# Performance work log

Measured on AMD Instinct MI355X. Metric: run time of the kernel, lower is better.

The kernel has to match this reference:

```python
import jax, jax.numpy as jnp
import numpy as np

H = 56; W = 56; WS = 7; SS = 3; NH = 6; C = 192; B = 32
T = H * W; HD = C // NH; NW = (H // WS) * (W // WS); TW = WS * WS
SCALE = HD ** -0.5


def _rel_index():
    # relative position index per WindowAttentionLayer.calculate_coordinates
    coords = np.stack(np.meshgrid(np.arange(WS), np.arange(WS), indexing='ij')).reshape(2, -1)
    rel = (coords[:, :, None] - coords[:, None, :]).transpose(1, 2, 0).astype(np.int64)
    rel[:, :, 0] += WS - 1
    rel[:, :, 1] += WS - 1
    rel[:, :, 0] *= 2 * WS - 1
    return rel.sum(-1).reshape(-1)  # [TW*TW]


def _attn_mask():
    # shifted-window attention mask, per WindowAttentionBlock.__init__
    img = np.zeros((H, W))
    slices = (slice(0, -WS), slice(-WS, -SS), slice(-SS, None))
    cnt = 0
    for hs in slices:
        for ws_ in slices:
            img[hs, ws_] = cnt
            cnt += 1
    mw = img.reshape(H // WS, WS, W // WS, WS).transpose(0, 2, 1, 3).reshape(-1, TW)
    am = mw[:, None, :] - mw[:, :, None]
    return np.where(am != 0, np.float32(-100.0), np.float32(0.0))  # [NW, TW, TW]


_REL = jnp.asarray(_rel_index())
_MASK = jnp.asarray(_attn_mask())


def _ln(x, g, b):
    m = x.mean(-1, keepdims=True)
    v = ((x - m) ** 2).mean(-1, keepdims=True)
    return (x - m) * jax.lax.rsqrt(v + 1e-5) * g + b


def setup_inputs() -> dict:
    key = jax.random.key(0)
    ks = jax.random.split(key, 8)
    s = 0.02
    return {
        'x': jax.random.normal(ks[0], (B, T, C), jnp.float32),
        'ln1_g': jnp.ones((C,), jnp.float32),
        'ln1_b': jnp.zeros((C,), jnp.float32),
        'qkv_w': jax.random.normal(ks[1], (C, 3 * C), jnp.float32) * s,
        'qkv_b': jnp.zeros((3 * C,), jnp.float32),
        'pos_bias': jax.random.normal(ks[2], ((2 * WS - 1) * (2 * WS - 1), NH), jnp.float32) * s,
        'proj_w': jax.random.normal(ks[3], (C, C), jnp.float32) * s,
        'proj_b': jnp.zeros((C,), jnp.float32),
        'ln2_g': jnp.ones((C,), jnp.float32),
        'ln2_b': jnp.zeros((C,), jnp.float32),
        'mlp_w1': jax.random.normal(ks[4], (C, 4 * C), jnp.float32) * s,
        'mlp_b1': jnp.zeros((4 * C,), jnp.float32),
        'mlp_w2': jax.random.normal(ks[5], (4 * C, C), jnp.float32) * s,
        'mlp_b2': jnp.zeros((C,), jnp.float32),
    }


def reference(x, ln1_g, ln1_b, qkv_w, qkv_b, pos_bias, proj_w, proj_b,
              ln2_g, ln2_b, mlp_w1, mlp_b1, mlp_w2, mlp_b2):
    shortcut = x
    h = _ln(x, ln1_g, ln1_b).reshape(B, H, W, C)
    h = jnp.roll(h, (-SS, -SS), axis=(1, 2))  # cyclic shift
    # window partition -> [B*NW, TW, C]
    h = h.reshape(B, H // WS, WS, W // WS, WS, C).transpose(0, 1, 3, 2, 4, 5).reshape(B * NW, TW, C)
    qkv = (h @ qkv_w + qkv_b).reshape(B * NW, TW, 3, NH, HD).transpose(2, 0, 3, 1, 4)
    q, k, v = qkv[0] * SCALE, qkv[1], qkv[2]  # [B*NW, NH, TW, HD]
    attn = jnp.einsum('nhid,nhjd->nhij', q, k)  # [B*NW, NH, TW, TW]
    bias = pos_bias[_REL].reshape(TW, TW, NH).transpose(2, 0, 1)  # [NH, TW, TW]
    attn = attn + bias[None]
    attn = (attn.reshape(B, NW, NH, TW, TW) + _MASK[None, :, None]).reshape(B * NW, NH, TW, TW)
    # NOTE: the source forward never applies softmax (self.softmax is unused) -- replicated faithfully
    o = jnp.einsum('nhij,nhjd->nhid', attn, v).transpose(0, 2, 1, 3).reshape(B * NW, TW, C)
    o = o @ proj_w + proj_b
    # window reverse + reverse shift
    o = o.reshape(B, H // WS, W // WS, WS, WS, C).transpose(0, 1, 3, 2, 4, 5).reshape(B, H, W, C)
    o = jnp.roll(o, (SS, SS), axis=(1, 2)).reshape(B, T, C)
    x1 = shortcut + o
    m = _ln(x1, ln2_g, ln2_b)
    m = jax.nn.gelu(m @ mlp_w1 + mlp_b1, approximate=False) @ mlp_w2 + mlp_b2
    return x1 + m
```

## Files before the change

kernel.cpp:

```cpp
#include <hip/hip_runtime.h>
#include <hip/hip_bf16.h>

typedef __attribute__((ext_vector_type(8))) short short8;
typedef __attribute__((ext_vector_type(4))) float floatx4;

#define SCALE_Q 0.17677669529663687f

__device__ __forceinline__ short f2bf(float f) {
  union { float f; unsigned u; } a; a.f = f;
  unsigned r = (a.u + 0x7FFFu + ((a.u >> 16) & 1u)) >> 16;
  return (short)r;
}

__device__ __forceinline__ int spatial_row(int r) {
  int n = r / 49, tw = r - n * 49;
  int bb = n >> 6, wdx = n & 63;
  int rh = (wdx >> 3) * 7 + tw / 7, rw = (wdx & 7) * 7 + tw % 7;
  int oh = rh + 3; if (oh >= 56) oh -= 56;
  int ow = rw + 3; if (ow >= 56) ow -= 56;
  return bb * 3136 + oh * 56 + ow;
}

__global__ void transpose_w_k(const float* __restrict__ src, short* __restrict__ dst,
                              int K, int N) {
  int i = blockIdx.x * 256 + threadIdx.x;
  if (i >= N * K) return;
  int n = i / K, k = i - n * K;
  dst[i] = f2bf(src[(size_t)k * N + n]);
}

__global__ void prep_bm_k(const float* __restrict__ pos_bias, float* __restrict__ bm) {
  int i = blockIdx.x * 256 + threadIdx.x;
  if (i >= 64 * 6 * 49 * 49) return;
  int j = i % 49; int t = i / 49; int ii = t % 49; t /= 49; int h = t % 6; int w = t / 6;
  int ih = ii / 7, iw = ii - ih * 7, jh = j / 7, jw = j - jh * 7;
  int rel = (ih - jh + 6) * 13 + (iw - jw + 6);
  float v = pos_bias[rel * 6 + h];
  int wh = w >> 3, ww = w & 7;
  int ri = wh * 7 + ih, ci = ww * 7 + iw, rj = wh * 7 + jh, cj = ww * 7 + jw;
  int regi = ((ri >= 49) + (ri >= 53)) * 3 + ((ci >= 49) + (ci >= 53));
  int regj = ((rj >= 49) + (rj >= 53)) * 3 + ((cj >= 49) + (cj >= 53));
  if (regi != regj) v -= 100.0f;
  bm[i] = v;
}

__global__ __launch_bounds__(256) void ln_k(const float* __restrict__ x,
    const float* __restrict__ g, const float* __restrict__ bta,
    short* __restrict__ outb) {
  int wid = threadIdx.x >> 6, lane = threadIdx.x & 63;
  int r = blockIdx.x * 4 + wid;
  int n = r / 49, tw = r - n * 49;
  int bb = n >> 6, wdx = n & 63;
  int rh = (wdx >> 3) * 7 + tw / 7, rw = (wdx & 7) * 7 + tw % 7;
  int sh = rh + 3; if (sh >= 56) sh -= 56;
  int sw = rw + 3; if (sw >= 56) sw -= 56;
  size_t src = ((size_t)bb * 3136 + sh * 56 + sw) * 192;
  const float* xr = x + src;
  float v0 = xr[lane], v1 = xr[lane + 64], v2 = xr[lane + 128];
  float s = v0 + v1 + v2, sq = v0 * v0 + v1 * v1 + v2 * v2;
  #pragma unroll
  for (int o = 32; o >= 1; o >>= 1) { s += __shfl_xor(s, o); sq += __shfl_xor(sq, o); }
  float mean = s * (1.0f / 192.0f);
  float rstd = rsqrtf(sq * (1.0f / 192.0f) - mean * mean + 1e-5f);
  short* orow = outb + (size_t)r * 192;
  orow[lane]       = f2bf((v0 - mean) * rstd * g[lane]       + bta[lane]);
  orow[lane + 64]  = f2bf((v1 - mean) * rstd * g[lane + 64]  + bta[lane + 64]);
  orow[lane + 128] = f2bf((v2 - mean) * rstd * g[lane + 128] + bta[lane + 128]);
}

__global__ __launch_bounds__(256) void gemm_qkv_k(
    const short* __restrict__ A, const short* __restrict__ Bt,
    const float* __restrict__ bias, short* __restrict__ outp, int N, int K) {
  __shared__ short As[128][72];
  __shared__ short Bs[64][72];
  int tid = threadIdx.x;
  int gmb = blockIdx.y * 128;
  int gnb = blockIdx.x * 64;
  int wid = tid >> 6, lane = tid & 63;
  int wm = wid >> 1, wn = wid & 1;
  int lr = lane & 15, lk = (lane >> 4) << 3, lq = (lane >> 4) << 2;
  floatx4 acc[4][2];
  #pragma unroll
  for (int i = 0; i < 4; ++i)
    #pragma unroll
    for (int j = 0; j < 2; ++j) acc[i][j] = (floatx4)(0.0f);

  for (int k0 = 0; k0 < K; k0 += 64) {
    #pragma unroll
    for (int i = 0; i < 4; ++i) {
      int u = tid + 256 * i;
      int row = u >> 3, cb = (u & 7) << 3;
      *(short8*)&As[row][cb] = *(const short8*)&A[(size_t)(gmb + row) * K + k0 + cb];
    }
    #pragma unroll
    for (int i = 0; i < 2; ++i) {
      int u = tid + 256 * i;
      int row = u >> 3, cb = (u & 7) << 3;
      *(short8*)&Bs[row][cb] = *(const short8*)&Bt[(size_t)(gnb + row) * K + k0 + cb];
    }
    __syncthreads();
    #pragma unroll
    for (int kk = 0; kk < 64; kk += 32) {
      short8 af[4], bfr[2];
      #pragma unroll
      for (int mi = 0; mi < 4; ++mi)
        af[mi] = *(const short8*)&As[wm * 64 + mi * 16 + lr][kk + lk];
      #pragma unroll
      for (int ni = 0; ni < 2; ++ni)
        bfr[ni] = *(const short8*)&Bs[wn * 32 + ni * 16 + lr][kk + lk];
      #pragma unroll
      for (int mi = 0; mi < 4; ++mi)
        #pragma unroll
        for (int ni = 0; ni < 2; ++ni)
          acc[mi][ni] = __builtin_amdgcn_mfma_f32_16x16x32_bf16(af[mi], bfr[ni], acc[mi][ni], 0, 0, 0);
    }
    __syncthreads();
  }

  #pragma unroll
  for (int mi = 0; mi < 4; ++mi)
    #pragma unroll
    for (int ni = 0; ni < 2; ++ni)
      #pragma unroll
      for (int r = 0; r < 4; ++r) {
        int grow = gmb + wm * 64 + mi * 16 + lq + r;
        int gcol = gnb + wn * 32 + ni * 16 + lr;
        float v = acc[mi][ni][r] + bias[gcol];
        int which = gcol / 192, rem = gcol - which * 192;
        if (which == 0) v *= SCALE_Q;
        int head = rem >> 5, d = rem & 31;
        int n = grow / 49, tw = grow - n * 49;
        outp[((((size_t)(n * 6 + head) * 3 + which) * 49 + tw) << 5) + d] = f2bf(v);
      }
}

__global__ __launch_bounds__(256) void attn_k(const short* __restrict__ qkv,
    const float* __restrict__ bm, short* __restrict__ obuf) {
  __shared__ short lds[4][6912];
  int wid = threadIdx.x >> 6, lane = threadIdx.x & 63;
  int pair = blockIdx.x * 4 + wid;
  int n = pair / 6, h = pair - n * 6;
  short* Vt = &lds[wid][0];
  short* Ps = &lds[wid][32 * 72];
  const short* Qb = qkv + (size_t)((n * 6 + h) * 3) * 1568;
  const short* Kb = Qb + 1568;
  const short* Vb = Qb + 3136;
  int lr = lane & 15, lk = (lane >> 4) << 3, lq = (lane >> 4) << 2;

  #pragma unroll
  for (int it = 0; it < 8; ++it) {
    int u = lane + 64 * it;
    Vt[(u >> 4) * 72 + 48 + (u & 15)] = 0;
  }
  #pragma unroll
  for (int it = 0; it < 4; ++it) {
    int u = lane + 64 * it;
    if (u < 196) {
      int tw = u >> 2, db = (u & 3) << 3;
      short8 vv = *(const short8*)&Vb[tw * 32 + db];
      #pragma unroll
      for (int j = 0; j < 8; ++j) Vt[(db + j) * 72 + tw] = vv[j];
    }
  }

  short8 qf[4], kf[4];
  #pragma unroll
  for (int mi = 0; mi < 4; ++mi)
    qf[mi] = *(const short8*)&Qb[(mi * 16 + lr) * 32 + lk];
  #pragma unroll
  for (int nj = 0; nj < 4; ++nj)
    kf[nj] = *(const short8*)&Kb[(nj * 16 + lr) * 32 + lk];
  floatx4 s[4][4];
  #pragma unroll
  for (int mi = 0; mi < 4; ++mi)
    #pragma unroll
    for (int nj = 0; nj < 4; ++nj)
      s[mi][nj] = __builtin_amdgcn_mfma_f32_16x16x32_bf16(qf[mi], kf[nj], (floatx4)(0.0f), 0, 0, 0);

  const float* bmw = bm + (size_t)((n & 63) * 6 + h) * 2401;
  #pragma unroll
  for (int mi = 0; mi < 4; ++mi)
    #pragma unroll
    for (int nj = 0; nj < 4; ++nj)
      #pragma unroll
      for (int r = 0; r < 4; ++r) {
        int i = mi * 16 + lq + r;
        int j = nj * 16 + lr;
        float v = 0.0f;
        if (i < 49 && j < 49) v = s[mi][nj][r] + bmw[i * 49 + j];
        Ps[i * 72 + j] = f2bf(v);
      }

  floatx4 o[4][2];
  #pragma unroll
  for (int mi = 0; mi < 4; ++mi)
    #pragma unroll
    for (int ni = 0; ni < 2; ++ni) o[mi][ni] = (floatx4)(0.0f);
  #pragma unroll
  for (int kc = 0; kc < 2; ++kc) {
    short8 pf[4], vf[2];
    #pragma unroll
    for (int mi = 0; mi < 4; ++mi)
      pf[mi] = *(const short8*)&Ps[(mi * 16 + lr) * 72 + kc * 32 + lk];
    #pragma unroll
    for (int ni = 0; ni < 2; ++ni)
      vf[ni] = *(const short8*)&Vt[(ni * 16 + lr) * 72 + kc * 32 + lk];
    #pragma unroll
    for (int mi = 0; mi < 4; ++mi)
      #pragma unroll
      for (int ni = 0; ni < 2; ++ni)
        o[mi][ni] = __builtin_amdgcn_mfma_f32_16x16x32_bf16(pf[mi], vf[ni], o[mi][ni], 0, 0, 0);
  }
  #pragma unroll
  for (int mi = 0; mi < 4; ++mi)
    #pragma unroll
    for (int ni = 0; ni < 2; ++ni)
      #pragma unroll
      for (int r = 0; r < 4; ++r) {
        int i = mi * 16 + lq + r;
        if (i < 49)
          obuf[((size_t)n * 49 + i) * 192 + h * 32 + ni * 16 + lr] = f2bf(o[mi][ni][r]);
      }
}

__global__ __launch_bounds__(512, 2) void tail_k(
    const short* __restrict__ obuf, const short* __restrict__ projT,
    const float* __restrict__ proj_b, const float* __restrict__ x,
    const float* __restrict__ g2, const float* __restrict__ bt2,
    const short* __restrict__ w1T, const float* __restrict__ b1,
    const short* __restrict__ w2T, const float* __restrict__ b2,
    float* __restrict__ out) {
  __shared__ short As[128][200];
  __shared__ short Hc[128][72];
  __shared__ float sums[128][4][2];
  __shared__ float stats[128][2];

  int tid = threadIdx.x;
  int wid = tid >> 6, lane = tid & 63;
  int wm = wid >> 2, wn = wid & 3;
  int lr = lane & 15, lk = (lane >> 4) << 3, lq = (lane >> 4) << 2;
  int blk = blockIdx.x * 128;

  floatx4 acc[4][3];
  #pragma unroll
  for (int mi = 0; mi < 4; ++mi)
    #pragma unroll
    for (int ni = 0; ni < 3; ++ni) acc[mi][ni] = (floatx4)(0.0f);
  #pragma unroll
  for (int kk = 0; kk < 6; ++kk) {
    short8 af[4], bfr[3];
    #pragma unroll
    for (int mi = 0; mi < 4; ++mi)
      af[mi] = *(const short8*)&obuf[(size_t)(blk + wm * 64 + mi * 16 + lr) * 192 + kk * 32 + lk];
    #pragma unroll
    for (int ni = 0; ni < 3; ++ni)
      bfr[ni] = *(const short8*)&projT[(size_t)(wn * 48 + ni * 16 + lr) * 192 + kk * 32 + lk];
    #pragma unroll
    for (int mi = 0; mi < 4; ++mi)
      #pragma unroll
      for (int ni = 0; ni < 3; ++ni)
        acc[mi][ni] = __builtin_amdgcn_mfma_f32_16x16x32_bf16(af[mi], bfr[ni], acc[mi][ni], 0, 0, 0);
  }

  float pb[3], gv[3], bv[3], pb2[3];
  int col[3];
  #pragma unroll
  for (int ni = 0; ni < 3; ++ni) {
    col[ni] = wn * 48 + ni * 16 + lr;
    pb[ni] = proj_b[col[ni]];
    gv[ni] = g2[col[ni]];
    bv[ni] = bt2[col[ni]];
    pb2[ni] = b2[col[ni]];
  }

  int srw[4][4];
  #pragma unroll
  for (int mi = 0; mi < 4; ++mi) {
    #pragma unroll
    for (int rr = 0; rr < 4; ++rr) {
      int row_l = wm * 64 + mi * 16 + lq + rr;
      int sr = spatial_row(blk + row_l);
      srw[mi][rr] = sr;
      float s = 0.0f, sq = 0.0f;
      #pragma unroll
      for (int ni = 0; ni < 3; ++ni) {
        float v = acc[mi][ni][rr] + pb[ni] + x[(size_t)sr * 192 + col[ni]];
        acc[mi][ni][rr] = v;
        s += v; sq += v * v;
      }
      #pragma unroll
      for (int o = 8; o >= 1; o >>= 1) { s += __shfl_xor(s, o); sq += __shfl_xor(sq, o); }
      if (lr == 0) { sums[row_l][wn][0] = s; sums[row_l][wn][1] = sq; }
    }
  }
  __syncthreads();
  if (tid < 128) {
    float s = sums[tid][0][0] + sums[tid][1][0] + sums[tid][2][0] + sums[tid][3][0];
    float sq = sums[tid][0][1] + sums[tid][1][1] + sums[tid][2][1] + sums[tid][3][1];
    float mean = s * (1.0f / 192.0f);
    float var = sq * (1.0f / 192.0f) - mean * mean;
    stats[tid][0] = mean;
    stats[tid][1] = rsqrtf(var + 1e-5f);
  }
  __syncthreads();

  #pragma unroll
  for (int mi = 0; mi < 4; ++mi)
    #pragma unroll
    for (int rr = 0; rr < 4; ++rr) {
      int row_l = wm * 64 + mi * 16 + lq + rr;
      float mean = stats[row_l][0], rstd = stats[row_l][1];
      #pragma unroll
      for (int ni = 0; ni < 3; ++ni)
        As[row_l][col[ni]] = f2bf((acc[mi][ni][rr] - mean) * rstd * gv[ni] + bv[ni]);
    }
  __syncthreads();

  int hcol = wn * 16 + lr;
  for (int c = 0; c < 12; ++c) {
    floatx4 hacc[4];
    #pragma unroll
    for (int mi = 0; mi < 4; ++mi) hacc[mi] = (floatx4)(0.0f);
    const short* w1p = w1T + (size_t)(c * 64 + hcol) * 192;
    #pragma unroll
    for (int kk = 0; kk < 6; ++kk) {
      short8 bfr = *(const short8*)&w1p[kk * 32 + lk];
      short8 af[4];
      #pragma unroll
      for (int mi = 0; mi < 4; ++mi)
        af[mi] = *(const short8*)&As[wm * 64 + mi * 16 + lr][kk * 32 + lk];
      #pragma unroll
      for (int mi = 0; mi < 4; ++mi)
        hacc[mi] = __builtin_amdgcn_mfma_f32_16x16x32_bf16(af[mi], bfr, hacc[mi], 0, 0, 0);
    }
    float b1v = b1[c * 64 + hcol];
    #pragma unroll
    for (int mi = 0; mi < 4; ++mi)
      #pragma unroll
      for (int rr = 0; rr < 4; ++rr) {
        float hv = hacc[mi][rr] + b1v;
        float ge = 0.5f * hv * (1.0f + erff(hv * 0.70710678118f));
        Hc[wm * 64 + mi * 16 + lq + rr][hcol] = f2bf(ge);
      }
    __syncthreads();
    #pragma unroll
    for (int kk = 0; kk < 2; ++kk) {
      short8 af[4], bfr[3];
      #pragma unroll
      for (int mi = 0; mi < 4; ++mi)
        af[mi] = *(const short8*)&Hc[wm * 64 + mi * 16 + lr][kk * 32 + lk];
      #pragma unroll
      for (int ni = 0; ni < 3; ++ni)
        bfr[ni] = *(const short8*)&w2T[(size_t)col[ni] * 768 + c * 64 + kk * 32 + lk];
      #pragma unroll
      for (int mi = 0; mi < 4; ++mi)
        #pragma unroll
        for (int ni = 0; ni < 3; ++ni)
          acc[mi][ni] = __builtin_amdgcn_mfma_f32_16x16x32_bf16(af[mi], bfr[ni], acc[mi][ni], 0, 0, 0);
    }
    __syncthreads();
  }

  #pragma unroll
  for (int mi = 0; mi < 4; ++mi)
    #pragma unroll
    for (int rr = 0; rr < 4; ++rr) {
      int sr = srw[mi][rr];
      #pragma unroll
      for (int ni = 0; ni < 3; ++ni)
        out[(size_t)sr * 192 + col[ni]] = acc[mi][ni][rr] + pb2[ni];
    }
}

extern "C" void kernel_launch(void* const* d_in, const int* in_sizes, int n_in,
                              void* d_out, int out_size, void* d_ws, size_t ws_size,
                              hipStream_t stream) {
  const float* x      = (const float*)d_in[0];
  const float* ln1_g  = (const float*)d_in[1];
  const float* ln1_b  = (const float*)d_in[2];
  const float* qkv_w  = (const float*)d_in[3];
  const float* qkv_b  = (const float*)d_in[4];
  const float* pos_b  = (const float*)d_in[5];
  const float* proj_w = (const float*)d_in[6];
  const float* proj_b = (const float*)d_in[7];
  const float* ln2_g  = (const float*)d_in[8];
  const float* ln2_b  = (const float*)d_in[9];
  const float* mlp_w1 = (const float*)d_in[10];
  const float* mlp_b1 = (const float*)d_in[11];
  const float* mlp_w2 = (const float*)d_in[12];
  const float* mlp_b2 = (const float*)d_in[13];

  char* ws = (char*)d_ws;
  short* qkvbuf  = (short*)(ws);
  short* obuf    = (short*)(ws + 115605504);
  short* hbuf    = (short*)(ws + 154140672);
  short* wT      = (short*)(ws + 192675840);
  short* qkv_wT  = wT;
  short* proj_wT = wT + 110592;
  short* m1_wT   = wT + 110592 + 36864;
  short* m2_wT   = wT + 110592 + 36864 + 147456;
  float* bm      = (float*)(ws + 193560576);
  float* xout    = (float*)d_out;

  transpose_w_k<<<(110592 + 255) / 256, 256, 0, stream>>>(qkv_w,  qkv_wT, 192, 576);
  transpose_w_k<<<(36864  + 255) / 256, 256, 0, stream>>>(proj_w, proj_wT, 192, 192);
  transpose_w_k<<<(147456 + 255) / 256, 256, 0, stream>>>(mlp_w1, m1_wT,  192, 768);
  transpose_w_k<<<(147456 + 255) / 256, 256, 0, stream>>>(mlp_w2, m2_wT,  768, 192);
  prep_bm_k<<<(64 * 6 * 2401 + 255) / 256, 256, 0, stream>>>(pos_b, bm);

  ln_k<<<25088, 256, 0, stream>>>(x, ln1_g, ln1_b, hbuf);
  gemm_qkv_k<<<dim3(9, 784), 256, 0, stream>>>(hbuf, qkv_wT, qkv_b, qkvbuf, 576, 192);
  attn_k<<<3072, 256, 0, stream>>>(qkvbuf, bm, obuf);
  tail_k<<<784, 512, 0, stream>>>(obuf, proj_wT, proj_b, x, ln2_g, ln2_b,
                                  m1_wT, mlp_b1, m2_wT, mlp_b2, xout);
}
```

Measured before the change: 576.3 us.

## Split fused tail into proj+LN2 kernel and a separate MLP kernel

Breaks the single tail kernel (proj GEMM, residual, LN2, MLP) into two kernels. The first writes x1 in fp32 to the output and a bf16 LN2 result into the workspace, reusing the qkv buffer. The second runs the MLP over 64-row tiles with 256-thread blocks and adds the residual back into the output. The aim is higher occupancy and better wave balance from smaller blocks and more of them. The cost is an extra round trip to global memory for x1 and the LN2 activations, and the MLP rows are now in spatial order rather than window order.

```diff
diff --git a/kernel.cpp b/kernel.cpp
--- a/kernel.cpp
+++ b/kernel.cpp
@@ -223,67 +223,61 @@
       }
 }
 
-__global__ __launch_bounds__(512, 2) void tail_k(
+__global__ __launch_bounds__(256, 4) void proj_ln2_k(
     const short* __restrict__ obuf, const short* __restrict__ projT,
     const float* __restrict__ proj_b, const float* __restrict__ x,
     const float* __restrict__ g2, const float* __restrict__ bt2,
-    const short* __restrict__ w1T, const float* __restrict__ b1,
-    const short* __restrict__ w2T, const float* __restrict__ b2,
-    float* __restrict__ out) {
-  __shared__ short As[128][200];
-  __shared__ short Hc[128][72];
-  __shared__ float sums[128][4][2];
-  __shared__ float stats[128][2];
-
+    float* __restrict__ x1out, short* __restrict__ ln2out) {
+  __shared__ float sums[64][2][2];
+  __shared__ float stats[64][2];
   int tid = threadIdx.x;
   int wid = tid >> 6, lane = tid & 63;
-  int wm = wid >> 2, wn = wid & 3;
+  int wm = wid >> 1, wn = wid & 1;
   int lr = lane & 15, lk = (lane >> 4) << 3, lq = (lane >> 4) << 2;
-  int blk = blockIdx.x * 128;
-
-  floatx4 acc[4][3];
-  #pragma unroll
-  for (int mi = 0; mi < 4; ++mi)
-    #pragma unroll
-    for (int ni = 0; ni < 3; ++ni) acc[mi][ni] = (floatx4)(0.0f);
+  int R0 = blockIdx.x * 64;
+
+  floatx4 acc[2][6];
+  #pragma unroll
+  for (int mi = 0; mi < 2; ++mi)
+    #pragma unroll
+    for (int ni = 0; ni < 6; ++ni) acc[mi][ni] = (floatx4)(0.0f);
+
   #pragma unroll
   for (int kk = 0; kk < 6; ++kk) {
-    short8 af[4], bfr[3];
-    #pragma unroll
-    for (int mi = 0; mi < 4; ++mi)
-      af[mi] = *(const short8*)&obuf[(size_t)(blk + wm * 64 + mi * 16 + lr) * 192 + kk * 32 + lk];
-    #pragma unroll
-    for (int ni = 0; ni < 3; ++ni)
-      bfr[ni] = *(const short8*)&projT[(size_t)(wn * 48 + ni * 16 + lr) * 192 + kk * 32 + lk];
-    #pragma unroll
-    for (int mi = 0; mi < 4; ++mi)
-      #pragma unroll
-      for (int ni = 0; ni < 3; ++ni)
+    short8 af[2], bfr[6];
+    #pragma unroll
+    for (int mi = 0; mi < 2; ++mi)
+      af[mi] = *(const short8*)&obuf[(size_t)(R0 + wm * 32 + mi * 16 + lr) * 192 + kk * 32 + lk];
+    #pragma unroll
+    for (int ni = 0; ni < 6; ++ni)
+      bfr[ni] = *(const short8*)&projT[(size_t)(wn * 96 + ni * 16 + lr) * 192 + kk * 32 + lk];
+    #pragma unroll
+    for (int mi = 0; mi < 2; ++mi)
+      #pragma unroll
+      for (int ni = 0; ni < 6; ++ni)
         acc[mi][ni] = __builtin_amdgcn_mfma_f32_16x16x32_bf16(af[mi], bfr[ni], acc[mi][ni], 0, 0, 0);
   }
 
-  float pb[3], gv[3], bv[3], pb2[3];
-  int col[3];
-  #pragma unroll
-  for (int ni = 0; ni < 3; ++ni) {
-    col[ni] = wn * 48 + ni * 16 + lr;
+  int col[6]; float pb[6], gv[6], bv[6];
+  #pragma unroll
+  for (int ni = 0; ni < 6; ++ni) {
+    col[ni] = wn * 96 + ni * 16 + lr;
     pb[ni] = proj_b[col[ni]];
     gv[ni] = g2[col[ni]];
     bv[ni] = bt2[col[ni]];
-    pb2[ni] = b2[col[ni]];
-  }
-
-  int srw[4][4];
-  #pragma unroll
-  for (int mi = 0; mi < 4; ++mi) {
+  }
+
+  int srw[2][4];
+  #pragma unroll
+  for (int mi = 0; mi < 2; ++mi)
     #pragma unroll
     for (int rr = 0; rr < 4; ++rr) {
-      int row_l = wm * 64 + mi * 16 + lq + rr;
-      int sr = spatial_row(blk + row_l);
+      int row_l = wm * 32 + mi * 16 + lq + rr;
+      int sr = spatial_row(R0 + row_l);
       srw[mi][rr] = sr;
       float s = 0.0f, sq = 0.0f;
       #pragma unroll
-      for (int ni = 0; ni < 3; ++ni) {
+      for (int ni = 0; ni < 6; ++ni) {
         float v = acc[mi][ni][rr] + pb[ni] + x[(size_t)sr * 192 + col[ni]];
         acc[mi][ni][rr] = v;
         s += v; sq += v * v;
@@ -292,11 +286,10 @@
       for (int o = 8; o >= 1; o >>= 1) { s += __shfl_xor(s, o); sq += __shfl_xor(sq, o); }
       if (lr == 0) { sums[row_l][wn][0] = s; sums[row_l][wn][1] = sq; }
     }
-  }
   __syncthreads();
-  if (tid < 128) {
-    float s = sums[tid][0][0] + sums[tid][1][0] + sums[tid][2][0] + sums[tid][3][0];
-    float sq = sums[tid][0][1] + sums[tid][1][1] + sums[tid][2][1] + sums[tid][3][1];
+  if (tid < 64) {
+    float s = sums[tid][0][0] + sums[tid][1][0];
+    float sq = sums[tid][0][1] + sums[tid][1][1];
     float mean = s * (1.0f / 192.0f);
     float var = sq * (1.0f / 192.0f) - mean * mean;
     stats[tid][0] = mean;
@@ -305,70 +298,116 @@
   __syncthreads();
 
   #pragma unroll
-  for (int mi = 0; mi < 4; ++mi)
+  for (int mi = 0; mi < 2; ++mi)
     #pragma unroll
     for (int rr = 0; rr < 4; ++rr) {
-      int row_l = wm * 64 + mi * 16 + lq + rr;
+      int row_l = wm * 32 + mi * 16 + lq + rr;
+      int sr = srw[mi][rr];
       float mean = stats[row_l][0], rstd = stats[row_l][1];
       #pragma unroll
-      for (int ni = 0; ni < 3; ++ni)
-        As[row_l][col[ni]] = f2bf((acc[mi][ni][rr] - mean) * rstd * gv[ni] + bv[ni]);
-    }
+      for (int ni = 0; ni < 6; ++ni) {
+        float v = acc[mi][ni][rr];
+        x1out[(size_t)sr * 192 + col[ni]] = v;
+        ln2out[(size_t)sr * 192 + col[ni]] = f2bf((v - mean) * rstd * gv[ni] + bv[ni]);
+      }
+    }
+}
+
+__global__ __launch_bounds__(256, 4) void mlp_k(
+    const short* __restrict__ ln2b, const float* __restrict__ x1,
+    const short* __restrict__ w1T, const float* __restrict__ b1,
+    const short* __restrict__ w2T, const float* __restrict__ b2,
+    float* __restrict__ out) {
+  __shared__ short As[64][200];
+  __shared__ short Hc[64][72];
+  int tid = threadIdx.x;
+  int wid = tid >> 6, lane = tid & 63;
+  int wm = wid >> 1, wn = wid & 1;
+  int lr = lane & 15, lk = (lane >> 4) << 3, lq = (lane >> 4) << 2;
+  int R0 = blockIdx.x * 64;
+
+  #pragma unroll
+  for (int it = 0; it < 6; ++it) {
+    int u = tid + 256 * it;
+    int row = u / 24, cb = (u - row * 24) * 8;
+    *(short8*)&As[row][cb] = *(const short8*)&ln2b[(size_t)(R0 + row) * 192 + cb];
+  }
+
+  float b2v[6];
+  int col[6];
+  #pragma unroll
+  for (int ni = 0; ni < 6; ++ni) {
+    col[ni] = wn * 96 + ni * 16 + lr;
+    b2v[ni] = b2[col[ni]];
+  }
+
+  floatx4 acc[2][6];
+  #pragma unroll
+  for (int mi = 0; mi < 2; ++mi)
+    #pragma unroll
+    for (int ni = 0; ni < 6; ++ni) acc[mi][ni] = (floatx4)(0.0f);
   __syncthreads();
 
-  int hcol = wn * 16 + lr;
   for (int c = 0; c < 12; ++c) {
-    floatx4 hacc[4];
-    #pragma unroll
-    for (int mi = 0; mi < 4; ++mi) hacc[mi] = (floatx4)(0.0f);
-    const short* w1p = w1T + (size_t)(c * 64 + hcol) * 192;
+    floatx4 hacc[2][2];
+    #pragma unroll
+    for (int mi = 0; mi < 2; ++mi)
+      #pragma unroll
+      for (int si = 0; si < 2; ++si) hacc[mi][si] = (floatx4)(0.0f);
     #pragma unroll
     for (int kk = 0; kk < 6; ++kk) {
-      short8 bfr = *(const short8*)&w1p[kk * 32 + lk];
-      short8 af[4];
-      #pragma unroll
-      for (int mi = 0; mi < 4; ++mi)
-        af[mi] = *(const short8*)&As[wm * 64 + mi * 16 + lr][kk * 32 + lk];
-      #pragma unroll
-      for (int mi = 0; mi < 4; ++mi)
-        hacc[mi] = __builtin_amdgcn_mfma_f32_16x16x32_bf16(af[mi], bfr, hacc[mi], 0, 0, 0);
-    }
-    float b1v = b1[c * 64 + hcol];
-    #pragma unroll
-    for (int mi = 0; mi < 4; ++mi)
-      #pragma unroll
-      for (int rr = 0; rr < 4; ++rr) {
-        float hv = hacc[mi][rr] + b1v;
-        float ge = 0.5f * hv * (1.0f + erff(hv * 0.70710678118f));
-        Hc[wm * 64 + mi * 16 + lq + rr][hcol] = f2bf(ge);
-      }
+      short8 af[2], bf1[2];
+      #pragma unroll
+      for (int mi = 0; mi < 2; ++mi)
+        af[mi] = *(const short8*)&As[wm * 32 + mi * 16 + lr][kk * 32 + lk];
+      #pragma unroll
+      for (int si = 0; si < 2; ++si)
+        bf1[si] = *(const short8*)&w1T[(size_t)(c * 64 + wn * 32 + si * 16 + lr) * 192 + kk * 32 + lk];
+      #pragma unroll
+      for (int mi = 0; mi < 2; ++mi)
+        #pragma unroll
+        for (int si = 0; si < 2; ++si)
+          hacc[mi][si] = __builtin_amdgcn_mfma_f32_16x16x32_bf16(af[mi], bf1[si], hacc[mi][si], 0, 0, 0);
+    }
+    #pragma unroll
+    for (int si = 0; si < 2; ++si) {
+      float b1v = b1[c * 64 + wn * 32 + si * 16 + lr];
+      #pragma unroll
+      for (int mi = 0; mi < 2; ++mi)
+        #pragma unroll
+        for (int rr = 0; rr < 4; ++rr) {
+          float hv = hacc[mi][si][rr] + b1v;
+          float ge = 0.5f * hv * (1.0f + erff(hv * 0.70710678118f));
+          Hc[wm * 32 + mi * 16 + lq + rr][wn * 32 + si * 16 + lr] = f2bf(ge);
+        }
+    }
     __syncthreads();
     #pragma unroll
     for (int kk = 0; kk < 2; ++kk) {
-      short8 af[4], bfr[3];
-      #pragma unroll
-      for (int mi = 0; mi < 4; ++mi)
-        af[mi] = *(const short8*)&Hc[wm * 64 + mi * 16 + lr][kk * 32 + lk];
-      #pragma unroll
-      for (int ni = 0; ni < 3; ++ni)
-        bfr[ni] = *(const short8*)&w2T[(size_t)col[ni] * 768 + c * 64 + kk * 32 + lk];
-      #pragma unroll
-      for (int mi = 0; mi < 4; ++mi)
+      short8 ah[2], bf2[6];
+      #pragma unroll
+      for (int mi = 0; mi < 2; ++mi)
+        ah[mi] = *(const short8*)&Hc[wm * 32 + mi * 16 + lr][kk * 32 + lk];
+      #pragma unroll
+      for (int ni = 0; ni < 6; ++ni)
+        bf2[ni] = *(const short8*)&w2T[(size_t)col[ni] * 768 + c * 64 + kk * 32 + lk];
+      #pragma unroll
+      for (int mi = 0; mi < 2; ++mi)
         #pragma unroll
-        for (int ni = 0; ni < 3; ++ni)
-          acc[mi][ni] = __builtin_amdgcn_mfma_f32_16x16x32_bf16(af[mi], bfr[ni], acc[mi][ni], 0, 0, 0);
+        for (int ni = 0; ni < 6; ++ni)
+          acc[mi][ni] = __builtin_amdgcn_mfma_f32_16x16x32_bf16(ah[mi], bf2[ni], acc[mi][ni], 0, 0, 0);
     }
     __syncthreads();
   }
 
   #pragma unroll
-  for (int mi = 0; mi < 4; ++mi)
+  for (int mi = 0; mi < 2; ++mi)
     #pragma unroll
     for (int rr = 0; rr < 4; ++rr) {
-      int sr = srw[mi][rr];
-      #pragma unroll
-      for (int ni = 0; ni < 3; ++ni)
-        out[(size_t)sr * 192 + col[ni]] = acc[mi][ni][rr] + pb2[ni];
+      size_t r = (size_t)(R0 + wm * 32 + mi * 16 + lq + rr) * 192;
+      #pragma unroll
+      for (int ni = 0; ni < 6; ++ni)
+        out[r + col[ni]] = x1[r + col[ni]] + acc[mi][ni][rr] + b2v[ni];
     }
 }
 
@@ -392,6 +431,7 @@
 
   char* ws = (char*)d_ws;
   short* qkvbuf  = (short*)(ws);
+  short* ln2b    = (short*)(ws);
   short* obuf    = (short*)(ws + 115605504);
   short* hbuf    = (short*)(ws + 154140672);
   short* wT      = (short*)(ws + 192675840);
@@ -411,6 +451,6 @@
   ln_k<<<25088, 256, 0, stream>>>(x, ln1_g, ln1_b, hbuf);
   gemm_qkv_k<<<dim3(9, 784), 256, 0, stream>>>(hbuf, qkv_wT, qkv_b, qkvbuf, 576, 192);
   attn_k<<<3072, 256, 0, stream>>>(qkvbuf, bm, obuf);
-  tail_k<<<784, 512, 0, stream>>>(obuf, proj_wT, proj_b, x, ln2_g, ln2_b,
-                                  m1_wT, mlp_b1, m2_wT, mlp_b2, xout);
-}
+  proj_ln2_k<<<1568, 256, 0, stream>>>(obuf, proj_wT, proj_b, x, ln2_g, ln2_b, xout, ln2b);
+  mlp_k<<<1568, 256, 0, stream>>>(ln2b, xout, m1_wT, mlp_b1, m2_wT, mlp_b2, xout);
+}
```

Result: slower. 604.2 us (+4.9%).

## Split fused tail kernel into proj+LN2, MLP1 and MLP2 kernels with LDS-staged tiles

Applied to the files above, without the earlier changes.

Replaces the single fused projection+LN2+MLP tail kernel with three kernels: projection with residual and LN2 writing x1 and bf16 LN output, a tiled MLP1 GEMM with GELU writing a bf16 hidden buffer, and a tiled MLP2 GEMM adding the residual. Each GEMM now stages A and B tiles in shared memory instead of reading weight fragments straight from global memory per wave. The MLP1 grid gains parallelism over the hidden dimension. In exchange it adds a round trip of the 768-wide hidden activation and of x1 through global memory, plus extra launches.

```diff
diff --git a/kernel.cpp b/kernel.cpp
--- a/kernel.cpp
+++ b/kernel.cpp
@@ -223,63 +223,75 @@
       }
 }
 
-__global__ __launch_bounds__(512, 2) void tail_k(
+__global__ __launch_bounds__(512) void proj_ln2_k(
     const short* __restrict__ obuf, const short* __restrict__ projT,
     const float* __restrict__ proj_b, const float* __restrict__ x,
     const float* __restrict__ g2, const float* __restrict__ bt2,
-    const short* __restrict__ w1T, const float* __restrict__ b1,
-    const short* __restrict__ w2T, const float* __restrict__ b2,
-    float* __restrict__ out) {
-  __shared__ short As[128][200];
-  __shared__ short Hc[128][72];
+    float* __restrict__ x1out, short* __restrict__ ln2out) {
+  __shared__ short As[128][72];
+  __shared__ short Bs[192][72];
   __shared__ float sums[128][4][2];
   __shared__ float stats[128][2];
-
   int tid = threadIdx.x;
   int wid = tid >> 6, lane = tid & 63;
   int wm = wid >> 2, wn = wid & 3;
   int lr = lane & 15, lk = (lane >> 4) << 3, lq = (lane >> 4) << 2;
-  int blk = blockIdx.x * 128;
+  int R0 = blockIdx.x * 128;
 
   floatx4 acc[4][3];
   #pragma unroll
   for (int mi = 0; mi < 4; ++mi)
     #pragma unroll
     for (int ni = 0; ni < 3; ++ni) acc[mi][ni] = (floatx4)(0.0f);
-  #pragma unroll
-  for (int kk = 0; kk < 6; ++kk) {
-    short8 af[4], bfr[3];
-    #pragma unroll
-    for (int mi = 0; mi < 4; ++mi)
-      af[mi] = *(const short8*)&obuf[(size_t)(blk + wm * 64 + mi * 16 + lr) * 192 + kk * 32 + lk];
-    #pragma unroll
-    for (int ni = 0; ni < 3; ++ni)
-      bfr[ni] = *(const short8*)&projT[(size_t)(wn * 48 + ni * 16 + lr) * 192 + kk * 32 + lk];
-    #pragma unroll
-    for (int mi = 0; mi < 4; ++mi)
+
+  for (int k0 = 0; k0 < 192; k0 += 64) {
+    #pragma unroll
+    for (int i = 0; i < 2; ++i) {
+      int u = tid + 512 * i;
+      int row = u >> 3, cb = (u & 7) << 3;
+      *(short8*)&As[row][cb] = *(const short8*)&obuf[(size_t)(R0 + row) * 192 + k0 + cb];
+    }
+    #pragma unroll
+    for (int i = 0; i < 3; ++i) {
+      int u = tid + 512 * i;
+      int row = u >> 3, cb = (u & 7) << 3;
+      *(short8*)&Bs[row][cb] = *(const short8*)&projT[(size_t)row * 192 + k0 + cb];
+    }
+    __syncthreads();
+    #pragma unroll
+    for (int kk = 0; kk < 64; kk += 32) {
+      short8 af[4], bfr[3];
+      #pragma unroll
+      for (int mi = 0; mi < 4; ++mi)
+        af[mi] = *(const short8*)&As[wm * 64 + mi * 16 + lr][kk + lk];
       #pragma unroll
       for (int ni = 0; ni < 3; ++ni)
-        acc[mi][ni] = __builtin_amdgcn_mfma_f32_16x16x32_bf16(af[mi], bfr[ni], acc[mi][ni], 0, 0, 0);
-  }
-
-  float pb[3], gv[3], bv[3], pb2[3];
-  int col[3];
+        bfr[ni] = *(const short8*)&Bs[wn * 48 + ni * 16 + lr][kk + lk];
+      #pragma unroll
+      for (int mi = 0; mi < 4; ++mi)
+        #pragma unroll
+        for (int ni = 0; ni < 3; ++ni)
+          acc[mi][ni] = __builtin_amdgcn_mfma_f32_16x16x32_bf16(af[mi], bfr[ni], acc[mi][ni], 0, 0, 0);
+    }
+    __syncthreads();
+  }
+
+  int col[3]; float pb[3], gv[3], bv[3];
   #pragma unroll
   for (int ni = 0; ni < 3; ++ni) {
     col[ni] = wn * 48 + ni * 16 + lr;
     pb[ni] = proj_b[col[ni]];
     gv[ni] = g2[col[ni]];
     bv[ni] = bt2[col[ni]];
-    pb2[ni] = b2[col[ni]];
   }
 
   int srw[4][4];
   #pragma unroll
-  for (int mi = 0; mi < 4; ++mi) {
+  for (int mi = 0; mi < 4; ++mi)
     #pragma unroll
     for (int rr = 0; rr < 4; ++rr) {
       int row_l = wm * 64 + mi * 16 + lq + rr;
-      int sr = spatial_row(blk + row_l);
+      int sr = spatial_row(R0 + row_l);
       srw[mi][rr] = sr;
       float s = 0.0f, sq = 0.0f;
       #pragma unroll
@@ -292,7 +304,6 @@
       for (int o = 8; o >= 1; o >>= 1) { s += __shfl_xor(s, o); sq += __shfl_xor(sq, o); }
       if (lr == 0) { sums[row_l][wn][0] = s; sums[row_l][wn][1] = sq; }
     }
-  }
   __syncthreads();
   if (tid < 128) {
     float s = sums[tid][0][0] + sums[tid][1][0] + sums[tid][2][0] + sums[tid][3][0];
@@ -309,49 +320,119 @@
     #pragma unroll
     for (int rr = 0; rr < 4; ++rr) {
       int row_l = wm * 64 + mi * 16 + lq + rr;
+      int sr = srw[mi][rr];
       float mean = stats[row_l][0], rstd = stats[row_l][1];
       #pragma unroll
+      for (int ni = 0; ni < 3; ++ni) {
+        float v = acc[mi][ni][rr];
+        x1out[(size_t)sr * 192 + col[ni]] = v;
+        ln2out[(size_t)sr * 192 + col[ni]] = f2bf((v - mean) * rstd * gv[ni] + bv[ni]);
+      }
+    }
+}
+
+__global__ __launch_bounds__(512) void mlp1_k(
+    const short* __restrict__ A, const short* __restrict__ w1T,
+    const float* __restrict__ b1, short* __restrict__ hidden) {
+  __shared__ short As[128][72];
+  __shared__ short Bs[128][72];
+  int tid = threadIdx.x;
+  int wid = tid >> 6, lane = tid & 63;
+  int wm = wid >> 2, wn = wid & 3;
+  int lr = lane & 15, lk = (lane >> 4) << 3, lq = (lane >> 4) << 2;
+  int R0 = blockIdx.y * 128;
+  int N0 = blockIdx.x * 128;
+
+  floatx4 acc[4][2];
+  #pragma unroll
+  for (int mi = 0; mi < 4; ++mi)
+    #pragma unroll
+    for (int ni = 0; ni < 2; ++ni) acc[mi][ni] = (floatx4)(0.0f);
+
+  for (int k0 = 0; k0 < 192; k0 += 64) {
+    #pragma unroll
+    for (int i = 0; i < 2; ++i) {
+      int u = tid + 512 * i;
+      int row = u >> 3, cb = (u & 7) << 3;
+      *(short8*)&As[row][cb] = *(const short8*)&A[(size_t)(R0 + row) * 192 + k0 + cb];
+      *(short8*)&Bs[row][cb] = *(const short8*)&w1T[(size_t)(N0 + row) * 192 + k0 + cb];
+    }
+    __syncthreads();
+    #pragma unroll
+    for (int kk = 0; kk < 64; kk += 32) {
+      short8 af[4], bfr[2];
+      #pragma unroll
+      for (int mi = 0; mi < 4; ++mi)
+        af[mi] = *(const short8*)&As[wm * 64 + mi * 16 + lr][kk + lk];
+      #pragma unroll
+      for (int ni = 0; ni < 2; ++ni)
+        bfr[ni] = *(const short8*)&Bs[wn * 32 + ni * 16 + lr][kk + lk];
+      #pragma unroll
+      for (int mi = 0; mi < 4; ++mi)
+        #pragma unroll
+        for (int ni = 0; ni < 2; ++ni)
+          acc[mi][ni] = __builtin_amdgcn_mfma_f32_16x16x32_bf16(af[mi], bfr[ni], acc[mi][ni], 0, 0, 0);
+    }
+    __syncthreads();
+  }
+
+  #pragma unroll
+  for (int ni = 0; ni < 2; ++ni) {
+    int gcol = N0 + wn * 32 + ni * 16 + lr;
+    float b1v = b1[gcol];
+    #pragma unroll
+    for (int mi = 0; mi < 4; ++mi)
+      #pragma unroll
+      for (int rr = 0; rr < 4; ++rr) {
+        int grow = R0 + wm * 64 + mi * 16 + lq + rr;
+        float hv = acc[mi][ni][rr] + b1v;
+        float ge = 0.5f * hv * (1.0f + erff(hv * 0.70710678118f));
+        hidden[(size_t)grow * 768 + gcol] = f2bf(ge);
+      }
+  }
+}
+
+__global__ __launch_bounds__(512) void mlp2_k(
+    const short* __restrict__ hidden, const float* __restrict__ x1,
+    const short* __restrict__ w2T, const float* __restrict__ b2,
+    float* __restrict__ out) {
+  __shared__ short As[128][72];
+  __shared__ short Bs[192][72];
+  int tid = threadIdx.x;
+  int wid = tid >> 6, lane = tid & 63;
+  int wm = wid >> 2, wn = wid & 3;
+  int lr = lane & 15, lk = (lane >> 4) << 3, lq = (lane >> 4) << 2;
+  int R0 = blockIdx.x * 128;
+
+  floatx4 acc[4][3];
+  #pragma unroll
+  for (int mi = 0; mi < 4; ++mi)
+    #pragma unroll
+    for (int ni = 0; ni < 3; ++ni) acc[mi][ni] = (floatx4)(0.0f);
+
+  for (int k0 = 0; k0 < 768; k0 += 64) {
+    #pragma unroll
+    for (int i = 0; i < 2; ++i) {
+      int u = tid + 512 * i;
+      int row = u >> 3, cb = (u & 7) << 3;
+      *(short8*)&As[row][cb] = *(const short8*)&hidden[(size_t)(R0 + row) * 768 + k0 + cb];
+    }
+    #pragma unroll
+    for (int i = 0; i < 3; ++i) {
+      int u = tid + 512 * i;
+      int row = u >> 3, cb = (u & 7) << 3;
+      *(short8*)&Bs[row][cb] = *(const short8*)&w2T[(size_t)row * 768 + k0 + cb];
+    }
+    __syncthreads();
+    #pragma unroll
+    for (int kk = 0; kk < 64; kk += 32) {
+      short8 af[4], bfr[3];
+      #pragma unroll
+      for (int mi = 0; mi < 4; ++mi)
+        af[mi] = *(const short8*)&As[wm * 64 + mi * 16 + lr][kk + lk];
+      #pragma unroll
       for (int ni = 0; ni < 3; ++ni)
-        As[row_l][col[ni]] = f2bf((acc[mi][ni][rr] - mean) * rstd * gv[ni] + bv[ni]);
-    }
-  __syncthreads();
-
-  int hcol = wn * 16 + lr;
-  for (int c = 0; c < 12; ++c) {
-    floatx4 hacc[4];
-    #pragma unroll
-    for (int mi = 0; mi < 4; ++mi) hacc[mi] = (floatx4)(0.0f);
-    const short* w1p = w1T + (size_t)(c * 64 + hcol) * 192;
-    #pragma unroll
-    for (int kk = 0; kk < 6; ++kk) {
-      short8 bfr = *(const short8*)&w1p[kk * 32 + lk];
-      short8 af[4];
-      #pragma unroll
-      for (int mi = 0; mi < 4; ++mi)
-        af[mi] = *(const short8*)&As[wm * 64 + mi * 16 + lr][kk * 32 + lk];
-      #pragma unroll
-      for (int mi = 0; mi < 4; ++mi)
-        hacc[mi] = __builtin_amdgcn_mfma_f32_16x16x32_bf16(af[mi], bfr, hacc[mi], 0, 0, 0);
-    }
-    float b1v = b1[c * 64 + hcol];
-    #pragma unroll
-    for (int mi = 0; mi < 4; ++mi)
-      #pragma unroll
-      for (int rr = 0; rr < 4; ++rr) {
-        float hv = hacc[mi][rr] + b1v;
-        float ge = 0.5f * hv * (1.0f + erff(hv * 0.70710678118f));
-        Hc[wm * 64 + mi * 16 + lq + rr][hcol] = f2bf(ge);
-      }
-    __syncthreads();
-    #pragma unroll
-    for (int kk = 0; kk < 2; ++kk) {
-      short8 af[4], bfr[3];
-      #pragma unroll
-      for (int mi = 0; mi < 4; ++mi)
-        af[mi] = *(const short8*)&Hc[wm * 64 + mi * 16 + lr][kk * 32 + lk];
-      #pragma unroll
-      for (int ni = 0; ni < 3; ++ni)
-        bfr[ni] = *(const short8*)&w2T[(size_t)col[ni] * 768 + c * 64 + kk * 32 + lk];
+        bfr[ni] = *(const short8*)&Bs[wn * 48 + ni * 16 + lr][kk + lk];
       #pragma unroll
       for (int mi = 0; mi < 4; ++mi)
         #pragma unroll
@@ -362,14 +443,17 @@
   }
 
   #pragma unroll
-  for (int mi = 0; mi < 4; ++mi)
-    #pragma unroll
-    for (int rr = 0; rr < 4; ++rr) {
-      int sr = srw[mi][rr];
-      #pragma unroll
-      for (int ni = 0; ni < 3; ++ni)
-        out[(size_t)sr * 192 + col[ni]] = acc[mi][ni][rr] + pb2[ni];
-    }
+  for (int ni = 0; ni < 3; ++ni) {
+    int gcol = wn * 48 + ni * 16 + lr;
+    float b2v = b2[gcol];
+    #pragma unroll
+    for (int mi = 0; mi < 4; ++mi)
+      #pragma unroll
+      for (int rr = 0; rr < 4; ++rr) {
+        size_t r = (size_t)(R0 + wm * 64 + mi * 16 + lq + rr) * 192;
+        out[r + gcol] = x1[r + gcol] + acc[mi][ni][rr] + b2v;
+      }
+  }
 }
 
 extern "C" void kernel_launch(void* const* d_in, const int* in_sizes, int n_in,
@@ -392,8 +476,10 @@
 
   char* ws = (char*)d_ws;
   short* qkvbuf  = (short*)(ws);
+  short* hidden  = (short*)(ws);
   short* obuf    = (short*)(ws + 115605504);
   short* hbuf    = (short*)(ws + 154140672);
+  short* ln2b    = (short*)(ws + 154140672);
   short* wT      = (short*)(ws + 192675840);
   short* qkv_wT  = wT;
   short* proj_wT = wT + 110592;
@@ -411,6 +497,7 @@
   ln_k<<<25088, 256, 0, stream>>>(x, ln1_g, ln1_b, hbuf);
   gemm_qkv_k<<<dim3(9, 784), 256, 0, stream>>>(hbuf, qkv_wT, qkv_b, qkvbuf, 576, 192);
   attn_k<<<3072, 256, 0, stream>>>(qkvbuf, bm, obuf);
-  tail_k<<<784, 512, 0, stream>>>(obuf, proj_wT, proj_b, x, ln2_g, ln2_b,
-                                  m1_wT, mlp_b1, m2_wT, mlp_b2, xout);
-}
+  proj_ln2_k<<<784, 512, 0, stream>>>(obuf, proj_wT, proj_b, x, ln2_g, ln2_b, xout, ln2b);
+  mlp1_k<<<dim3(6, 784), 512, 0, stream>>>(ln2b, m1_wT, mlp_b1, hidden);
+  mlp2_k<<<784, 512, 0, stream>>>(hidden, xout, m2_wT, mlp_b2, xout);
+}
```

Result: faster. 530.0 us (-8.0%).

## Split fused MLP tail into separate pipelined GEMM kernels with register prefetch

Applied to the files above, without the earlier changes.

Breaks up the fused proj+LN2+MLP tail kernel. The proj+LN2 kernel now stages operands through LDS and writes x1 (fp32) and the LN2 output (bf16) to global memory. The MLP then runs as two generic tiled GEMM launches: one with a GELU epilogue writing the hidden activations, one with a residual-add epilogue. All GEMMs gain register prefetch of the next K tile, overlapping global loads with MFMA work. This removes the serialized 12-chunk inner loop and its per-chunk syncs, but adds global round-trips for the 768-wide hidden tensor, the LN2 output and x1.

```diff
diff --git a/kernel.cpp b/kernel.cpp
--- a/kernel.cpp
+++ b/kernel.cpp
@@ -68,9 +68,11 @@
   orow[lane + 128] = f2bf((v2 - mean) * rstd * g[lane + 128] + bta[lane + 128]);
 }
 
-__global__ __launch_bounds__(256) void gemm_qkv_k(
+template<int EPI>
+__global__ __launch_bounds__(256) void pgemm_k(
     const short* __restrict__ A, const short* __restrict__ Bt,
-    const float* __restrict__ bias, short* __restrict__ outp, int N, int K) {
+    const float* __restrict__ bias, void* __restrict__ outp,
+    const void* __restrict__ aux, int N, int K) {
   __shared__ short As[128][72];
   __shared__ short Bs[64][72];
   int tid = threadIdx.x;
@@ -79,26 +81,36 @@
   int wid = tid >> 6, lane = tid & 63;
   int wm = wid >> 1, wn = wid & 1;
   int lr = lane & 15, lk = (lane >> 4) << 3, lq = (lane >> 4) << 2;
+  int ar = tid >> 3, ac = (tid & 7) << 3;
+
   floatx4 acc[4][2];
   #pragma unroll
   for (int i = 0; i < 4; ++i)
     #pragma unroll
     for (int j = 0; j < 2; ++j) acc[i][j] = (floatx4)(0.0f);
 
+  short8 pa[4], pb[2];
+  #pragma unroll
+  for (int i = 0; i < 4; ++i)
+    pa[i] = *(const short8*)&A[(size_t)(gmb + ar + 32 * i) * K + ac];
+  #pragma unroll
+  for (int i = 0; i < 2; ++i)
+    pb[i] = *(const short8*)&Bt[(size_t)(gnb + ar + 32 * i) * K + ac];
+
   for (int k0 = 0; k0 < K; k0 += 64) {
     #pragma unroll
-    for (int i = 0; i < 4; ++i) {
-      int u = tid + 256 * i;
-      int row = u >> 3, cb = (u & 7) << 3;
-      *(short8*)&As[row][cb] = *(const short8*)&A[(size_t)(gmb + row) * K + k0 + cb];
-    }
-    #pragma unroll
-    for (int i = 0; i < 2; ++i) {
-      int u = tid + 256 * i;
-      int row = u >> 3, cb = (u & 7) << 3;
-      *(short8*)&Bs[row][cb] = *(const short8*)&Bt[(size_t)(gnb + row) * K + k0 + cb];
-    }
+    for (int i = 0; i < 4; ++i) *(short8*)&As[ar + 32 * i][ac] = pa[i];
+    #pragma unroll
+    for (int i = 0; i < 2; ++i) *(short8*)&Bs[ar + 32 * i][ac] = pb[i];
     __syncthreads();
+    if (k0 + 64 < K) {
+      #pragma unroll
+      for (int i = 0; i < 4; ++i)
+        pa[i] = *(const short8*)&A[(size_t)(gmb + ar + 32 * i) * K + k0 + 64 + ac];
+      #pragma unroll
+      for (int i = 0; i < 2; ++i)
+        pb[i] = *(const short8*)&Bt[(size_t)(gnb + ar + 32 * i) * K + k0 + 64 + ac];
+    }
     #pragma unroll
     for (int kk = 0; kk < 64; kk += 32) {
       short8 af[4], bfr[2];
@@ -126,11 +138,19 @@
         int grow = gmb + wm * 64 + mi * 16 + lq + r;
         int gcol = gnb + wn * 32 + ni * 16 + lr;
         float v = acc[mi][ni][r] + bias[gcol];
-        int which = gcol / 192, rem = gcol - which * 192;
-        if (which == 0) v *= SCALE_Q;
-        int head = rem >> 5, d = rem & 31;
-        int n = grow / 49, tw = grow - n * 49;
-        outp[((((size_t)(n * 6 + head) * 3 + which) * 49 + tw) << 5) + d] = f2bf(v);
+        if (EPI == 0) {
+          int which = gcol / 192, rem = gcol - which * 192;
+          if (which == 0) v *= SCALE_Q;
+          int head = rem >> 5, d = rem & 31;
+          int n = grow / 49, tw = grow - n * 49;
+          ((short*)outp)[((((size_t)(n * 6 + head) * 3 + which) * 49 + tw) << 5) + d] = f2bf(v);
+        } else if (EPI == 2) {
+          float ge = 0.5f * v * (1.0f + erff(v * 0.70710678118f));
+          ((short*)outp)[(size_t)grow * 768 + gcol] = f2bf(ge);
+        } else {
+          size_t idx = (size_t)grow * 192 + gcol;
+          ((float*)outp)[idx] = ((const float*)aux)[idx] + v;
+        }
       }
 }
 
@@ -223,63 +243,84 @@
       }
 }
 
-__global__ __launch_bounds__(512, 2) void tail_k(
+__global__ __launch_bounds__(512) void proj_ln2_k(
     const short* __restrict__ obuf, const short* __restrict__ projT,
     const float* __restrict__ proj_b, const float* __restrict__ x,
     const float* __restrict__ g2, const float* __restrict__ bt2,
-    const short* __restrict__ w1T, const float* __restrict__ b1,
-    const short* __restrict__ w2T, const float* __restrict__ b2,
-    float* __restrict__ out) {
-  __shared__ short As[128][200];
-  __shared__ short Hc[128][72];
+    float* __restrict__ x1out, short* __restrict__ ln2out) {
+  __shared__ short As[128][72];
+  __shared__ short Bs[192][72];
   __shared__ float sums[128][4][2];
   __shared__ float stats[128][2];
-
   int tid = threadIdx.x;
   int wid = tid >> 6, lane = tid & 63;
   int wm = wid >> 2, wn = wid & 3;
   int lr = lane & 15, lk = (lane >> 4) << 3, lq = (lane >> 4) << 2;
-  int blk = blockIdx.x * 128;
+  int R0 = blockIdx.x * 128;
+  int ar = tid >> 3, ac = (tid & 7) << 3;
 
   floatx4 acc[4][3];
   #pragma unroll
   for (int mi = 0; mi < 4; ++mi)
     #pragma unroll
     for (int ni = 0; ni < 3; ++ni) acc[mi][ni] = (floatx4)(0.0f);
-  #pragma unroll
-  for (int kk = 0; kk < 6; ++kk) {
-    short8 af[4], bfr[3];
-    #pragma unroll
-    for (int mi = 0; mi < 4; ++mi)
-      af[mi] = *(const short8*)&obuf[(size_t)(blk + wm * 64 + mi * 16 + lr) * 192 + kk * 32 + lk];
-    #pragma unroll
-    for (int ni = 0; ni < 3; ++ni)
-      bfr[ni] = *(const short8*)&projT[(size_t)(wn * 48 + ni * 16 + lr) * 192 + kk * 32 + lk];
-    #pragma unroll
-    for (int mi = 0; mi < 4; ++mi)
+
+  short8 pa[2], pbr[3];
+  #pragma unroll
+  for (int i = 0; i < 2; ++i)
+    pa[i] = *(const short8*)&obuf[(size_t)(R0 + ar + 64 * i) * 192 + ac];
+  #pragma unroll
+  for (int i = 0; i < 3; ++i)
+    pbr[i] = *(const short8*)&projT[(size_t)(ar + 64 * i) * 192 + ac];
+
+  for (int k0 = 0; k0 < 192; k0 += 64) {
+    #pragma unroll
+    for (int i = 0; i < 2; ++i) *(short8*)&As[ar + 64 * i][ac] = pa[i];
+    #pragma unroll
+    for (int i = 0; i < 3; ++i) *(short8*)&Bs[ar + 64 * i][ac] = pbr[i];
+    __syncthreads();
+    if (k0 < 128) {
+      #pragma unroll
+      for (int i = 0; i < 2; ++i)
+        pa[i] = *(const short8*)&obuf[(size_t)(R0 + ar + 64 * i) * 192 + k0 + 64 + ac];
+      #pragma unroll
+      for (int i = 0; i < 3; ++i)
+        pbr[i] = *(const short8*)&projT[(size_t)(ar + 64 * i) * 192 + k0 + 64 + ac];
+    }
+    #pragma unroll
+    for (int kk = 0; kk < 64; kk += 32) {
+      short8 af[4], bfr[3];
+      #pragma unroll
+      for (int mi = 0; mi < 4; ++mi)
+        af[mi] = *(const short8*)&As[wm * 64 + mi * 16 + lr][kk + lk];
       #pragma unroll
       for (int ni = 0; ni < 3; ++ni)
-        acc[mi][ni] = __builtin_amdgcn_mfma_f32_16x16x32_bf16(af[mi], bfr[ni], acc[mi][ni], 0, 0, 0);
-  }
-
-  float pb[3], gv[3], bv[3], pb2[3];
-  int col[3];
+        bfr[ni] = *(const short8*)&Bs[wn * 48 + ni * 16 + lr][kk + lk];
+      #pragma unroll
+      for (int mi = 0; mi < 4; ++mi)
+        #pragma unroll
+        for (int ni = 0; ni < 3; ++ni)
+          acc[mi][ni] = __builtin_amdgcn_mfma_f32_16x16x32_bf16(af[mi], bfr[ni], acc[mi][ni], 0, 0, 0);
+    }
+    __syncthreads();
+  }
+
+  int col[3]; float pb[3], gv[3], bv[3];
   #pragma unroll
   for (int ni = 0; ni < 3; ++ni) {
     col[ni] = wn * 48 + ni * 16 + lr;
     pb[ni] = proj_b[col[ni]];
     gv[ni] = g2[col[ni]];
     bv[ni] = bt2[col[ni]];
-    pb2[ni] = b2[col[ni]];
   }
 
   int srw[4][4];
   #pragma unroll
-  for (int mi = 0; mi < 4; ++mi) {
+  for (int mi = 0; mi < 4; ++mi)
     #pragma unroll
     for (int rr = 0; rr < 4; ++rr) {
       int row_l = wm * 64 + mi * 16 + lq + rr;
-      int sr = spatial_row(blk + row_l);
+      int sr = spatial_row(R0 + row_l);
       srw[mi][rr] = sr;
       float s = 0.0f, sq = 0.0f;
       #pragma unroll
@@ -292,7 +333,6 @@
       for (int o = 8; o >= 1; o >>= 1) { s += __shfl_xor(s, o); sq += __shfl_xor(sq, o); }
       if (lr == 0) { sums[row_l][wn][0] = s; sums[row_l][wn][1] = sq; }
     }
-  }
   __syncthreads();
   if (tid < 128) {
     float s = sums[tid][0][0] + sums[tid][1][0] + sums[tid][2][0] + sums[tid][3][0];
@@ -309,66 +349,14 @@
     #pragma unroll
     for (int rr = 0; rr < 4; ++rr) {
       int row_l = wm * 64 + mi * 16 + lq + rr;
+      int sr = srw[mi][rr];
       float mean = stats[row_l][0], rstd = stats[row_l][1];
       #pragma unroll
-      for (int ni = 0; ni < 3; ++ni)
-        As[row_l][col[ni]] = f2bf((acc[mi][ni][rr] - mean) * rstd * gv[ni] + bv[ni]);
-    }
-  __syncthreads();
-
-  int hcol = wn * 16 + lr;
-  for (int c = 0; c < 12; ++c) {
-    floatx4 hacc[4];
-    #pragma unroll
-    for (int mi = 0; mi < 4; ++mi) hacc[mi] = (floatx4)(0.0f);
-    const short* w1p = w1T + (size_t)(c * 64 + hcol) * 192;
-    #pragma unroll
-    for (int kk = 0; kk < 6; ++kk) {
-      short8 bfr = *(const short8*)&w1p[kk * 32 + lk];
-      short8 af[4];
-      #pragma unroll
-      for (int mi = 0; mi < 4; ++mi)
-        af[mi] = *(const short8*)&As[wm * 64 + mi * 16 + lr][kk * 32 + lk];
-      #pragma unroll
-      for (int mi = 0; mi < 4; ++mi)
-        hacc[mi] = __builtin_amdgcn_mfma_f32_16x16x32_bf16(af[mi], bfr, hacc[mi], 0, 0, 0);
-    }
-    float b1v = b1[c * 64 + hcol];
-    #pragma unroll
-    for (int mi = 0; mi < 4; ++mi)
-      #pragma unroll
-      for (int rr = 0; rr < 4; ++rr) {
-        float hv = hacc[mi][rr] + b1v;
-        float ge = 0.5f * hv * (1.0f + erff(hv * 0.70710678118f));
-        Hc[wm * 64 + mi * 16 + lq + rr][hcol] = f2bf(ge);
+      for (int ni = 0; ni < 3; ++ni) {
+        float v = acc[mi][ni][rr];
+        x1out[(size_t)sr * 192 + col[ni]] = v;
+        ln2out[(size_t)sr * 192 + col[ni]] = f2bf((v - mean) * rstd * gv[ni] + bv[ni]);
       }
-    __syncthreads();
-    #pragma unroll
-    for (int kk = 0; kk < 2; ++kk) {
-      short8 af[4], bfr[3];
-      #pragma unroll
-      for (int mi = 0; mi < 4; ++mi)
-        af[mi] = *(const short8*)&Hc[wm * 64 + mi * 16 + lr][kk * 32 + lk];
-      #pragma unroll
-      for (int ni = 0; ni < 3; ++ni)
-        bfr[ni] = *(const short8*)&w2T[(size_t)col[ni] * 768 + c * 64 + kk * 32 + lk];
-      #pragma unroll
-      for (int mi = 0; mi < 4; ++mi)
-        #pragma unroll
-        for (int ni = 0; ni < 3; ++ni)
-          acc[mi][ni] = __builtin_amdgcn_mfma_f32_16x16x32_bf16(af[mi], bfr[ni], acc[mi][ni], 0, 0, 0);
-    }
-    __syncthreads();
-  }
-
-  #pragma unroll
-  for (int mi = 0; mi < 4; ++mi)
-    #pragma unroll
-    for (int rr = 0; rr < 4; ++rr) {
-      int sr = srw[mi][rr];
-      #pragma unroll
-      for (int ni = 0; ni < 3; ++ni)
-        out[(size_t)sr * 192 + col[ni]] = acc[mi][ni][rr] + pb2[ni];
     }
 }
 
@@ -392,8 +380,10 @@
 
   char* ws = (char*)d_ws;
   short* qkvbuf  = (short*)(ws);
+  short* hidden  = (short*)(ws);
   short* obuf    = (short*)(ws + 115605504);
   short* hbuf    = (short*)(ws + 154140672);
+  short* ln2b    = (short*)(ws + 154140672);
   short* wT      = (short*)(ws + 192675840);
   short* qkv_wT  = wT;
   short* proj_wT = wT + 110592;
@@ -409,8 +399,9 @@
   prep_bm_k<<<(64 * 6 * 2401 + 255) / 256, 256, 0, stream>>>(pos_b, bm);
 
   ln_k<<<25088, 256, 0, stream>>>(x, ln1_g, ln1_b, hbuf);
-  gemm_qkv_k<<<dim3(9, 784), 256, 0, stream>>>(hbuf, qkv_wT, qkv_b, qkvbuf, 576, 192);
+  pgemm_k<0><<<dim3(9, 784),  256, 0, stream>>>(hbuf, qkv_wT, qkv_b, qkvbuf, nullptr, 576, 192);
   attn_k<<<3072, 256, 0, stream>>>(qkvbuf, bm, obuf);
-  tail_k<<<784, 512, 0, stream>>>(obuf, proj_wT, proj_b, x, ln2_g, ln2_b,
-                                  m1_wT, mlp_b1, m2_wT, mlp_b2, xout);
-}
+  proj_ln2_k<<<784, 512, 0, stream>>>(obuf, proj_wT, proj_b, x, ln2_g, ln2_b, xout, ln2b);
+  pgemm_k<2><<<dim3(12, 784), 256, 0, stream>>>(ln2b, m1_wT, mlp_b1, hidden, nullptr, 768, 192);
+  pgemm_k<3><<<dim3(3, 784),  256, 0, stream>>>(hidden, m2_wT, mlp_b2, xout, xout, 192, 768);
+}
```

After: 498.6 us. 13.5% less time.
